# Kernel tuning notes

Hardware: AMD Instinct MI355X
Metric: run time of the kernel (lower is better)

The kernel has to match this reference:

```python
import jax, jax.numpy as jnp
import numpy as np

N = 200_000          # nodes
E = 6_400_000        # edges (avg degree 32)
U, T, C, G = 200_000, 20_000, 5_000, 10_000  # table sizes
DU, DT, DC, DG = 8, 8, 2, 8                  # embedding dims
IC, H, OC = 8, 16, 1                          # input/hidden/output channels


def setup_inputs() -> dict:
    key = jax.random.key(0)
    ks = jax.random.split(key, 24)
    # node type in {0,1,2,4}
    tcode = jnp.array([0, 1, 2, 4], dtype=jnp.int32)[jax.random.randint(ks[0], (N,), 0, 4)]
    # per-type in-range index (size lookup by type code; slot 3 unused)
    sizes = jnp.array([U, T, C, 1, G], dtype=jnp.float32)
    u = jax.random.uniform(ks[1], (N,))
    idx = jnp.floor(u * sizes[tcode]).astype(jnp.int32)
    known = jax.random.randint(ks[2], (N,), 0, 2).astype(jnp.int32)
    features = jnp.stack([idx, known, tcode], axis=1)  # [N, 3]
    edges = jax.random.randint(ks[3], (2, E), 0, N).astype(jnp.int32)
    label_masks = jax.random.randint(ks[4], (N,), 0, 2).astype(jnp.int32)

    def w(k, shape, s=0.1):
        return jax.random.normal(k, shape, dtype=jnp.float32) * s

    return {
        "edges": edges, "features": features, "label_masks": label_masks,
        "user_emb": w(ks[5], (U, DU)), "known_emb": w(ks[6], (2, DU)),
        "mask_emb": w(ks[7], (2, DU)), "cat_emb": w(ks[8], (C, DC)),
        "topic_emb": w(ks[9], (T, DT)), "group_emb": w(ks[10], (G, DG)),
        "user_W": w(ks[11], (DU, IC)), "user_b": jnp.zeros((IC,), jnp.float32),
        "mask_W": w(ks[12], (DU, IC)), "mask_b": jnp.zeros((IC,), jnp.float32),
        "cat_W": w(ks[13], (DC, IC)), "cat_b": jnp.zeros((IC,), jnp.float32),
        "topic_W": w(ks[14], (DT, IC)), "topic_b": jnp.zeros((IC,), jnp.float32),
        "group_W": w(ks[15], (DG, IC)), "group_b": jnp.zeros((IC,), jnp.float32),
        "W0": w(ks[16], (IC, H)), "b0": jnp.zeros((H,), jnp.float32),
        "W2": w(ks[17], (H, OC)), "b2": jnp.zeros((OC,), jnp.float32),
    }


def _assemble(features, label_masks, user_emb, known_emb, mask_emb, cat_emb,
              topic_emb, group_emb, user_W, user_b, mask_W, mask_b, cat_W, cat_b,
              topic_W, topic_b, group_W, group_b):
    idx, known, tcode = features[:, 0], features[:, 1], features[:, 2]
    relu = jax.nn.relu
    # proj = Sequential(ReLU, Linear): relu first, then linear
    user_f = relu(user_emb[jnp.clip(idx, 0, U - 1)] + known_emb[jnp.clip(known, 0, 1)]) @ user_W + user_b
    topic_f = relu(topic_emb[jnp.clip(idx, 0, T - 1)]) @ topic_W + topic_b
    cat_f = relu(cat_emb[jnp.clip(idx, 0, C - 1)]) @ cat_W + cat_b
    group_f = relu(group_emb[jnp.clip(idx, 0, G - 1)]) @ group_W + group_b
    t = tcode[:, None]
    x = jnp.where(t == 0, user_f,
        jnp.where(t == 1, topic_f,
        jnp.where(t == 2, cat_f,
        jnp.where(t == 4, group_f, 0.0))))
    mask_f = jax.nn.sigmoid(relu(mask_emb[label_masks]) @ mask_W + mask_b)
    return x * mask_f  # [N, IC]


def _gcn_norm(edges, n):
    # add self-loops, symmetric normalization (PyG GCNConv default)
    loops = jnp.arange(n, dtype=edges.dtype)
    row = jnp.concatenate([edges[0], loops])
    col = jnp.concatenate([edges[1], loops])
    deg = jax.ops.segment_sum(jnp.ones_like(col, dtype=jnp.float32), col, num_segments=n)
    dis = jnp.where(deg > 0, jax.lax.rsqrt(jnp.where(deg > 0, deg, 1.0)), 0.0)
    return row, col, dis[row] * dis[col]


def _gcn_conv(x, row, col, norm, W, b):
    h = x @ W                                   # [N, out]
    msg = norm[:, None] * h[row]                # gather + scale over edges
    out = jax.ops.segment_sum(msg, col, num_segments=x.shape[0])
    return out + b


def reference(edges, features, label_masks, user_emb, known_emb, mask_emb,
              cat_emb, topic_emb, group_emb, user_W, user_b, mask_W, mask_b,
              cat_W, cat_b, topic_W, topic_b, group_W, group_b, W0, b0, W2, b2):
    x = _assemble(features, label_masks, user_emb, known_emb, mask_emb, cat_emb,
                  topic_emb, group_emb, user_W, user_b, mask_W, mask_b, cat_W,
                  cat_b, topic_W, topic_b, group_W, group_b)
    row, col, norm = _gcn_norm(edges, x.shape[0])
    # Original forward applies layers[0] (relu) then layers[-1]; layers[1] is skipped.
    x = jax.nn.relu(_gcn_conv(x, row, col, norm, W0, b0))
    return _gcn_conv(x, row, col, norm, W2, b2)  # [N, 1]
```

## Files before the change

### kernel.cpp

```cpp
#include <hip/hip_runtime.h>
#include <math.h>

constexpr int NN = 200000;
constexpr int EE = 6400000;
constexpr int NB = (NN + 255) / 256;
constexpr int U_ = 200000, T_ = 20000, C_ = 5000, G_ = 10000;

constexpr int BSH2  = 9;
constexpr int BUCKN = 1 << BSH2;
constexpr int NBUCK = (NN + BUCKN - 1) / BUCKN;
constexpr int CAP   = 18432;
constexpr int CHUNK  = 8192;
constexpr int NCHUNK = (EE + CHUNK - 1) / CHUNK;
constexpr int PER    = (NCHUNK + 255) / 256;

__device__ __forceinline__ int clampi(int v, int lo, int hi){ return v < lo ? lo : (v > hi ? hi : v); }
__device__ __forceinline__ float reluf(float v){ return v > 0.f ? v : 0.f; }


__global__ __launch_bounds__(512) void k_hist(const int* __restrict__ edges,
                                              int* __restrict__ cntmat){
  __shared__ int h[NBUCK];
  int t = threadIdx.x;
  for (int i = t; i < NBUCK; i += 512) h[i] = 0;
  __syncthreads();
  int base = blockIdx.x * CHUNK;
  int n = min(CHUNK, EE - base);
  for (int k = t; k < n; k += 512)
    atomicAdd(&h[edges[EE + base + k] >> BSH2], 1);
  __syncthreads();
  for (int i = t; i < NBUCK; i += 512)
    cntmat[(size_t)blockIdx.x * NBUCK + i] = h[i];
}


__global__ void k_scan2(const int* __restrict__ cntmat, int* __restrict__ offT,
                        int* __restrict__ binCnt){
  __shared__ int sc[256];
  int t = threadIdx.x;
  int b = blockIdx.x;
  int v[PER];
  int loc = 0;
  #pragma unroll
  for (int j = 0; j < PER; j++){
    int c = t * PER + j;
    v[j] = (c < NCHUNK) ? cntmat[(size_t)c * NBUCK + b] : 0;
    loc += v[j];
  }
  sc[t] = loc; __syncthreads();
  for (int d = 1; d < 256; d <<= 1){
    int u = (t >= d) ? sc[t - d] : 0;
    __syncthreads();
    sc[t] += u;
    __syncthreads();
  }
  int run = b * CAP + sc[t] - loc;
  #pragma unroll
  for (int j = 0; j < PER; j++){
    int c = t * PER + j;
    if (c < NCHUNK){ offT[(size_t)b * NCHUNK + c] = run; run += v[j]; }
  }
  if (t == 255) binCnt[b] = sc[255];
}


__global__ __launch_bounds__(512) void k_binA3(const int* __restrict__ edges,
                                               const int* __restrict__ cntmat,
                                               const int* __restrict__ offT,
                                               int* __restrict__ bin){
  __shared__ int cur[NBUCK];
  __shared__ int dlt[NBUCK];
  __shared__ int wsum[8];
  __shared__ int stage[CHUNK];
  __shared__ unsigned short stageB[CHUNK];

  int t = threadIdx.x;
  int chunk = blockIdx.x;
  int my = (t < NBUCK) ? cntmat[(size_t)chunk * NBUCK + t] : 0;
  int lane = t & 63, wid = t >> 6;
  int incl = my;
  #pragma unroll
  for (int d = 1; d < 64; d <<= 1){
    int u = __shfl_up(incl, d);
    if (lane >= d) incl += u;
  }
  if (lane == 63) wsum[wid] = incl;
  __syncthreads();
  int wpre = 0;
  #pragma unroll
  for (int w = 0; w < 8; w++) wpre += (w < wid) ? wsum[w] : 0;
  int excl = wpre + incl - my;
  if (t < NBUCK){
    cur[t] = excl;
    dlt[t] = offT[(size_t)t * NCHUNK + chunk] - excl;
  }
  __syncthreads();
  int base = chunk * CHUNK;
  int n = min(CHUNK, EE - base);
  for (int k = t; k < n; k += 512){
    int c = edges[EE + base + k];
    int r = edges[base + k];
    int b = c >> BSH2;
    int p = atomicAdd(&cur[b], 1);
    stage[p]  = r | ((c & (BUCKN - 1)) << 18);
    stageB[p] = (unsigned short)b;
  }
  __syncthreads();
  for (int k = t; k < n; k += 512){
    int b = stageB[k];
    int addr = dlt[b] + k;
    if (addr < (b + 1) * CAP)
      bin[addr] = stage[k];
  }
}


__global__ __launch_bounds__(512) void k_binB2(
    const int* __restrict__ bin, const int* __restrict__ binCnt,
    int* __restrict__ off, int* __restrict__ deg, int* __restrict__ seg,
    double* __restrict__ dis, int* __restrict__ srow){
  __shared__ int hist[4 * BUCKN];
  __shared__ int sc[512];
  __shared__ int stage[CAP];
  int t = threadIdx.x;
  int b = blockIdx.x;
  int nb = b << BSH2;
  int nloc = min(BUCKN, NN - nb);
  int s0 = b * CAP;
  int cntb = min(binCnt[b], CAP);
  int s1 = s0 + cntb;

  hist[t] = 0; hist[t + 512] = 0; hist[t + 1024] = 0; hist[t + 1536] = 0;
  __syncthreads();
  for (int k = s0 + t; k < s1; k += 512){
    int w = bin[k];
    int key = ((w >> 18) << 2) | ((w & 0x3FFFF) >> 16);
    atomicAdd(&hist[key], 1);
  }
  __syncthreads();
  int h0 = hist[4*t], h1 = hist[4*t+1], h2 = hist[4*t+2], h3 = hist[4*t+3];
  int tot = h0 + h1 + h2 + h3;
  sc[t] = tot; __syncthreads();
  for (int d = 1; d < 512; d <<= 1){
    int u = (t >= d) ? sc[t - d] : 0;
    __syncthreads();
    sc[t] += u;
    __syncthreads();
  }
  int base = sc[t] - tot;
  if (t < nloc){
    off[nb + t] = s0 + base;
    deg[nb + t] = tot;
    seg[nb + t] = h0 | ((h0 + h1) << 10) | ((h0 + h1 + h2) << 20);
    dis[nb + t] = 1.0 / sqrt((double)(tot + 1));
  }
  __syncthreads();
  hist[4*t]     = base;
  hist[4*t + 1] = base + h0;
  hist[4*t + 2] = base + h0 + h1;
  hist[4*t + 3] = base + h0 + h1 + h2;
  __syncthreads();
  for (int k = s0 + t; k < s1; k += 512){
    int w = bin[k];
    int key = ((w >> 18) << 2) | ((w & 0x3FFFF) >> 16);
    int p = atomicAdd(&hist[key], 1);
    stage[p] = w & 0x3FFFF;
  }
  __syncthreads();
  for (int k = t; k < cntb; k += 512)
    srow[s0 + k] = stage[k];
}


__global__ void k_assemble(
    const int* __restrict__ features, const int* __restrict__ lmask,
    const float* __restrict__ user_emb, const float* __restrict__ known_emb,
    const float* __restrict__ mask_emb, const float* __restrict__ cat_emb,
    const float* __restrict__ topic_emb, const float* __restrict__ group_emb,
    const float* __restrict__ user_W, const float* __restrict__ user_b,
    const float* __restrict__ mask_W, const float* __restrict__ mask_b,
    const float* __restrict__ cat_W, const float* __restrict__ cat_b,
    const float* __restrict__ topic_W, const float* __restrict__ topic_b,
    const float* __restrict__ group_W, const float* __restrict__ group_b,
    const double* __restrict__ dis, float* __restrict__ xs1)
{
  __shared__ float s_userW[64], s_topicW[64], s_groupW[64], s_maskW[64];
  __shared__ float s_catW[16], s_knownE[16], s_maskE[16];
  __shared__ float s_userb[8], s_topicb[8], s_catb[8], s_groupb[8], s_maskb[8];
  int tid = threadIdx.x;
  if (tid < 64){ s_userW[tid]=user_W[tid]; s_topicW[tid]=topic_W[tid];
                 s_groupW[tid]=group_W[tid]; s_maskW[tid]=mask_W[tid]; }
  if (tid < 16){ s_catW[tid]=cat_W[tid]; s_knownE[tid]=known_emb[tid]; s_maskE[tid]=mask_emb[tid]; }
  if (tid < 8){ s_userb[tid]=user_b[tid]; s_topicb[tid]=topic_b[tid]; s_catb[tid]=cat_b[tid];
                s_groupb[tid]=group_b[tid]; s_maskb[tid]=mask_b[tid]; }
  __syncthreads();

  int i = blockIdx.x * 256 + tid;
  if (i >= NN) return;

  int idx   = features[3*i + 0];
  int known = features[3*i + 1];
  int tc    = features[3*i + 2];

  double x[8];
  #pragma unroll
  for (int k = 0; k < 8; k++) x[k] = 0.0;

  if (tc == 0){
    int id = clampi(idx, 0, U_-1);
    int kn = clampi(known, 0, 1);
    float a[8];
    #pragma unroll
    for (int d = 0; d < 8; d++) a[d] = reluf(user_emb[(size_t)id*8 + d] + s_knownE[kn*8 + d]);
    #pragma unroll
    for (int k = 0; k < 8; k++){
      double s = (double)s_userb[k];
      #pragma unroll
      for (int d = 0; d < 8; d++) s += (double)a[d] * (double)s_userW[d*8 + k];
      x[k] = s;
    }
  } else if (tc == 1){
    int id = clampi(idx, 0, T_-1);
    float a[8];
    #pragma unroll
    for (int d = 0; d < 8; d++) a[d] = reluf(topic_emb[(size_t)id*8 + d]);
    #pragma unroll
    for (int k = 0; k < 8; k++){
      double s = (double)s_topicb[k];
      #pragma unroll
      for (int d = 0; d < 8; d++) s += (double)a[d] * (double)s_topicW[d*8 + k];
      x[k] = s;
    }
  } else if (tc == 2){
    int id = clampi(idx, 0, C_-1);
    float a0 = reluf(cat_emb[(size_t)id*2 + 0]);
    float a1 = reluf(cat_emb[(size_t)id*2 + 1]);
    #pragma unroll
    for (int k = 0; k < 8; k++)
      x[k] = (double)s_catb[k] + (double)a0*(double)s_catW[k] + (double)a1*(double)s_catW[8 + k];
  } else if (tc == 4){
    int id = clampi(idx, 0, G_-1);
    float a[8];
    #pragma unroll
    for (int d = 0; d < 8; d++) a[d] = reluf(group_emb[(size_t)id*8 + d]);
    #pragma unroll
    for (int k = 0; k < 8; k++){
      double s = (double)s_groupb[k];
      #pragma unroll
      for (int d = 0; d < 8; d++) s += (double)a[d] * (double)s_groupW[d*8 + k];
      x[k] = s;
    }
  }

  int m = clampi(lmask[i], 0, 1);
  float me[8];
  #pragma unroll
  for (int d = 0; d < 8; d++) me[d] = reluf(s_maskE[m*8 + d]);
  double di = dis[i];
  float xo[8];
  #pragma unroll
  for (int k = 0; k < 8; k++){
    double s = (double)s_maskb[k];
    #pragma unroll
    for (int d = 0; d < 8; d++) s += (double)me[d] * (double)s_maskW[d*8 + k];
    double mf = 1.0 / (1.0 + exp(-s));
    xo[k] = (float)(di * x[k] * mf);
  }
  float4* xp = (float4*)(xs1 + (size_t)i * 8);
  xp[0] = make_float4(xo[0], xo[1], xo[2], xo[3]);
  xp[1] = make_float4(xo[4], xo[5], xo[6], xo[7]);
}


__global__ void k_agg1(const float* __restrict__ xs1, const int* __restrict__ srow,
                       const int* __restrict__ off, const int* __restrict__ cnt,
                       const int* __restrict__ seg, const double* __restrict__ dis,
                       const float* __restrict__ b0, const float* __restrict__ W0,
                       const float* __restrict__ W2, float* __restrict__ h2s)
{
  __shared__ float sW0[128], sb0[16], sW2[16];
  int tid = threadIdx.x;
  if (tid < 128) sW0[tid] = W0[tid];
  if (tid < 16){ sb0[tid] = b0[tid]; sW2[tid] = W2[tid]; }
  __syncthreads();

  int gid = blockIdx.x * 256 + tid;
  int i = gid >> 2, h = gid & 3;
  if (i >= NN) return;

  const float2* xp = (const float2*)xs1;
  float2 sv = xp[(size_t)i*4 + h];
  double a0 = sv.x, a1 = sv.y;
  int s = off[i], c = cnt[i], sg = seg[i];
  int bnd[5];
  bnd[0] = 0;
  bnd[1] = sg & 1023;
  bnd[2] = (sg >> 10) & 1023;
  bnd[3] = (sg >> 20) & 1023;
  bnd[4] = c;
  #pragma unroll 1
  for (int p = 0; p < 4; p++){
    int j = bnd[p], je = bnd[p + 1];
    for (; j + 4 <= je; j += 4){
      int r0 = srow[s+j], r1 = srow[s+j+1], r2 = srow[s+j+2], r3 = srow[s+j+3];
      float2 v0 = xp[(size_t)r0*4 + h], v1 = xp[(size_t)r1*4 + h],
             v2 = xp[(size_t)r2*4 + h], v3 = xp[(size_t)r3*4 + h];
      a0 += v0.x; a1 += v0.y;
      a0 += v1.x; a1 += v1.y;
      a0 += v2.x; a1 += v2.y;
      a0 += v3.x; a1 += v3.y;
    }
    for (; j < je; ++j){
      int r = srow[s + j];
      float2 v = xp[(size_t)r*4 + h];
      a0 += v.x; a1 += v.y;
    }
  }
  double e0 = __shfl_xor(a0, 1), e1 = __shfl_xor(a1, 1);
  double q0, q1, q2, q3;
  if ((h & 1) == 0){ q0 = a0; q1 = a1; q2 = e0; q3 = e1; }
  else             { q0 = e0; q1 = e1; q2 = a0; q3 = a1; }
  double f0 = __shfl_xor(q0, 2), f1 = __shfl_xor(q1, 2),
         f2 = __shfl_xor(q2, 2), f3 = __shfl_xor(q3, 2);
  double X[8];
  if ((h & 2) == 0){ X[0]=q0; X[1]=q1; X[2]=q2; X[3]=q3; X[4]=f0; X[5]=f1; X[6]=f2; X[7]=f3; }
  else             { X[0]=f0; X[1]=f1; X[2]=f2; X[3]=f3; X[4]=q0; X[5]=q1; X[6]=q2; X[7]=q3; }

  double di = dis[i];
  double h2p = 0.0;
  #pragma unroll
  for (int jj = 0; jj < 4; jj++){
    int j = h * 4 + jj;
    double t = 0.0;
    #pragma unroll
    for (int cc = 0; cc < 8; cc++) t += X[cc] * (double)sW0[cc*16 + j];
    t = di * t + (double)sb0[j];
    double x2 = t > 0.0 ? t : 0.0;
    h2p += x2 * (double)sW2[j];
  }
  h2p += __shfl_xor(h2p, 1);
  h2p += __shfl_xor(h2p, 2);
  if (h == 0) h2s[i] = (float)(di * h2p);
}


__global__ void k_agg2(const float* __restrict__ h2s, const int* __restrict__ srow,
                       const int* __restrict__ off, const int* __restrict__ cnt,
                       const double* __restrict__ dis, const float* __restrict__ b2,
                       float* __restrict__ out)
{
  int gid = blockIdx.x * 256 + threadIdx.x;
  int i = gid >> 2, h = gid & 3;
  if (i >= NN) return;
  double acc = (h == 0) ? (double)h2s[i] : 0.0;
  int s = off[i], c = cnt[i];
  for (int j = h; j < c; j += 4)
    acc += (double)h2s[srow[s + j]];
  acc += __shfl_xor(acc, 1);
  acc += __shfl_xor(acc, 2);
  if (h == 0) out[i] = (float)(dis[i] * acc + (double)b2[0]);
}


extern "C" void kernel_launch(void* const* d_in, const int* in_sizes, int n_in,
                              void* d_out, int out_size, void* d_ws, size_t ws_size,
                              hipStream_t stream)
{
  const int*   edges      = (const int*)  d_in[0];
  const int*   features   = (const int*)  d_in[1];
  const int*   label_mask = (const int*)  d_in[2];
  const float* user_emb   = (const float*)d_in[3];
  const float* known_emb  = (const float*)d_in[4];
  const float* mask_emb   = (const float*)d_in[5];
  const float* cat_emb    = (const float*)d_in[6];
  const float* topic_emb  = (const float*)d_in[7];
  const float* group_emb  = (const float*)d_in[8];
  const float* user_W     = (const float*)d_in[9];
  const float* user_b     = (const float*)d_in[10];
  const float* mask_W     = (const float*)d_in[11];
  const float* mask_b     = (const float*)d_in[12];
  const float* cat_W      = (const float*)d_in[13];
  const float* cat_b      = (const float*)d_in[14];
  const float* topic_W    = (const float*)d_in[15];
  const float* topic_b    = (const float*)d_in[16];
  const float* group_W    = (const float*)d_in[17];
  const float* group_b    = (const float*)d_in[18];
  const float* W0         = (const float*)d_in[19];
  const float* b0         = (const float*)d_in[20];
  const float* W2         = (const float*)d_in[21];
  const float* b2         = (const float*)d_in[22];
  float* out = (float*)d_out;

  char* ws = (char*)d_ws;
  size_t o = 0;
  auto alloc = [&](size_t bytes){ void* p = ws + o; o += (bytes + 255) & ~255ull; return p; };
  int*    cntmat = (int*)   alloc((size_t)NCHUNK * NBUCK * 4);
  int*    offT   = (int*)   alloc((size_t)NBUCK * NCHUNK * 4);
  int*    binCnt = (int*)   alloc((size_t)NBUCK * 4);
  int*    off    = (int*)   alloc((size_t)NN * 4);
  int*    deg    = (int*)   alloc((size_t)NN * 4);
  int*    seg    = (int*)   alloc((size_t)NN * 4);
  double* dis    = (double*)alloc((size_t)NN * 8);
  int*    srow   = (int*)   alloc((size_t)NBUCK * CAP * 4);
  int*    bin    = (int*)   alloc((size_t)NBUCK * CAP * 4);
  float*  xs1    = (float*) alloc((size_t)NN * 8 * 4);
  float*  h2s    = (float*) alloc((size_t)NN * 4);

  k_hist    <<<NCHUNK, 512, 0, stream>>>(edges, cntmat);
  k_scan2   <<<NBUCK,  256, 0, stream>>>(cntmat, offT, binCnt);
  k_binA3   <<<NCHUNK, 512, 0, stream>>>(edges, cntmat, offT, bin);
  k_binB2   <<<NBUCK,  512, 0, stream>>>(bin, binCnt, off, deg, seg, dis, srow);
  k_assemble<<<NB,     256, 0, stream>>>(features, label_mask,
      user_emb, known_emb, mask_emb, cat_emb, topic_emb, group_emb,
      user_W, user_b, mask_W, mask_b, cat_W, cat_b,
      topic_W, topic_b, group_W, group_b, dis, xs1);
  k_agg1    <<<(4*NN + 255)/256, 256, 0, stream>>>(xs1, srow, off, deg, seg, dis, b0, W0, W2, h2s);
  k_agg2    <<<(4*NN + 255)/256, 256, 0, stream>>>(h2s, srow, off, deg, dis, b2, out);
}
```

Before: 185.0 us.

## Sort neighbors into eight source-range groups and barrier-sync gather phases

Each destination's neighbor list is now sorted into eight source-index ranges instead of four, with per-group counts packed into two 8-bit-field words per node. The layer-1 aggregation walks the eight groups with a block-wide barrier after each one, so all threads in a block gather from the same region of the feature array at roughly the same time. The aim is better cache locality for the random gathers. The cost is a larger sort histogram, doubled seg storage, and barrier stalls when neighbor counts are uneven. The 8-bit fields overflow if a group holds more than 255 edges.

```diff
diff --git a/kernel.cpp b/kernel.cpp
--- a/kernel.cpp
+++ b/kernel.cpp
@@ -119,7 +119,7 @@
     const int* __restrict__ bin, const int* __restrict__ binCnt,
     int* __restrict__ off, int* __restrict__ deg, int* __restrict__ seg,
     double* __restrict__ dis, int* __restrict__ srow){
-  __shared__ int hist[4 * BUCKN];
+  __shared__ int hist[8 * BUCKN];
   __shared__ int sc[512];
   __shared__ int stage[CAP];
   int t = threadIdx.x;
@@ -130,16 +130,19 @@
   int cntb = min(binCnt[b], CAP);
   int s1 = s0 + cntb;
 
-  hist[t] = 0; hist[t + 512] = 0; hist[t + 1024] = 0; hist[t + 1536] = 0;
+  #pragma unroll
+  for (int q = 0; q < 8; q++) hist[t + 512*q] = 0;
   __syncthreads();
   for (int k = s0 + t; k < s1; k += 512){
     int w = bin[k];
-    int key = ((w >> 18) << 2) | ((w & 0x3FFFF) >> 16);
+    int key = ((w >> 18) << 3) | ((w & 0x3FFFF) >> 15);
     atomicAdd(&hist[key], 1);
   }
   __syncthreads();
-  int h0 = hist[4*t], h1 = hist[4*t+1], h2 = hist[4*t+2], h3 = hist[4*t+3];
-  int tot = h0 + h1 + h2 + h3;
+  int hv[8];
+  int tot = 0;
+  #pragma unroll
+  for (int q = 0; q < 8; q++){ hv[q] = hist[8*t + q]; tot += hv[q]; }
   sc[t] = tot; __syncthreads();
   for (int d = 1; d < 512; d <<= 1){
     int u = (t >= d) ? sc[t - d] : 0;
@@ -151,18 +154,18 @@
   if (t < nloc){
     off[nb + t] = s0 + base;
     deg[nb + t] = tot;
-    seg[nb + t] = h0 | ((h0 + h1) << 10) | ((h0 + h1 + h2) << 20);
+    seg[2*(nb + t)]     = hv[0] | (hv[1] << 8) | (hv[2] << 16) | (hv[3] << 24);
+    seg[2*(nb + t) + 1] = hv[4] | (hv[5] << 8) | (hv[6] << 16) | (hv[7] << 24);
     dis[nb + t] = 1.0 / sqrt((double)(tot + 1));
   }
   __syncthreads();
-  hist[4*t]     = base;
-  hist[4*t + 1] = base + h0;
-  hist[4*t + 2] = base + h0 + h1;
-  hist[4*t + 3] = base + h0 + h1 + h2;
+  int run = base;
+  #pragma unroll
+  for (int q = 0; q < 8; q++){ hist[8*t + q] = run; run += hv[q]; }
   __syncthreads();
   for (int k = s0 + t; k < s1; k += 512){
     int w = bin[k];
-    int key = ((w >> 18) << 2) | ((w & 0x3FFFF) >> 16);
+    int key = ((w >> 18) << 3) | ((w & 0x3FFFF) >> 15);
     int p = atomicAdd(&hist[key], 1);
     stage[p] = w & 0x3FFFF;
   }
@@ -286,20 +289,21 @@
 
   int gid = blockIdx.x * 256 + tid;
   int i = gid >> 2, h = gid & 3;
-  if (i >= NN) return;
 
   const float2* xp = (const float2*)xs1;
   float2 sv = xp[(size_t)i*4 + h];
   double a0 = sv.x, a1 = sv.y;
-  int s = off[i], c = cnt[i], sg = seg[i];
-  int bnd[5];
+  int s = off[i];
+  int sgA = seg[2*i], sgB = seg[2*i + 1];
+  int bnd[9];
   bnd[0] = 0;
-  bnd[1] = sg & 1023;
-  bnd[2] = (sg >> 10) & 1023;
-  bnd[3] = (sg >> 20) & 1023;
-  bnd[4] = c;
+  #pragma unroll
+  for (int g = 0; g < 4; g++) bnd[g+1] = bnd[g] + ((sgA >> (8*g)) & 255);
+  #pragma unroll
+  for (int g = 0; g < 4; g++) bnd[g+5] = bnd[g+4] + ((sgB >> (8*g)) & 255);
+
   #pragma unroll 1
-  for (int p = 0; p < 4; p++){
+  for (int p = 0; p < 8; p++){
     int j = bnd[p], je = bnd[p + 1];
     for (; j + 4 <= je; j += 4){
       int r0 = srow[s+j], r1 = srow[s+j+1], r2 = srow[s+j+2], r3 = srow[s+j+3];
@@ -315,6 +319,7 @@
       float2 v = xp[(size_t)r*4 + h];
       a0 += v.x; a1 += v.y;
     }
+    __syncthreads();
   }
   double e0 = __shfl_xor(a0, 1), e1 = __shfl_xor(a1, 1);
   double q0, q1, q2, q3;
@@ -399,7 +404,7 @@
   int*    binCnt = (int*)   alloc((size_t)NBUCK * 4);
   int*    off    = (int*)   alloc((size_t)NN * 4);
   int*    deg    = (int*)   alloc((size_t)NN * 4);
-  int*    seg    = (int*)   alloc((size_t)NN * 4);
+  int*    seg    = (int*)   alloc((size_t)NN * 8);
   double* dis    = (double*)alloc((size_t)NN * 8);
   int*    srow   = (int*)   alloc((size_t)NBUCK * CAP * 4);
   int*    bin    = (int*)   alloc((size_t)NBUCK * CAP * 4);
@@ -414,6 +419,6 @@
       user_emb, known_emb, mask_emb, cat_emb, topic_emb, group_emb,
       user_W, user_b, mask_W, mask_b, cat_W, cat_b,
       topic_W, topic_b, group_W, group_b, dis, xs1);
-  k_agg1    <<<(4*NN + 255)/256, 256, 0, stream>>>(xs1, srow, off, deg, seg, dis, b0, W0, W2, h2s);
+  k_agg1    <<<(4*NN)/256, 256, 0, stream>>>(xs1, srow, off, deg, seg, dis, b0, W0, W2, h2s);
   k_agg2    <<<(4*NN + 255)/256, 256, 0, stream>>>(h2s, srow, off, deg, dis, b2, out);
 }
```

After: 190.6 us. 1.03x slower.
